# Kernel optimization log

Measured on AMD Instinct MI355X. Metric: run time of the kernel, lower is better.

Reference implementation:

```python
import jax, jax.numpy as jnp
import numpy as np

B_, N_, D_ = 2, 2048, 512
E_ = 2 * D_          # d_inner = expand * dim
S_ = 16              # d_state
K_ = 4               # d_conv
R_ = 32              # dt_rank = ceil(dim/16)
C_ = 512             # cond_dim


def setup_inputs() -> dict:
    key = jax.random.key(0)
    ks = jax.random.split(key, 12)
    r = lambda i, sh, s=0.02: jax.random.normal(ks[i], sh, dtype=jnp.float32) * s
    return {
        "x": jax.random.normal(ks[0], (B_, N_, D_), dtype=jnp.float32),
        "cond": jax.random.normal(ks[1], (B_, C_), dtype=jnp.float32),
        "ln_g": jnp.ones((D_,), jnp.float32),
        "ln_b": jnp.zeros((D_,), jnp.float32),
        "W_in": r(2, (D_, 2 * E_)),            # in_proj (no bias)
        "conv_w": r(3, (E_, K_), 0.1),          # depthwise causal conv
        "conv_b": jnp.zeros((E_,), jnp.float32),
        "W_x": r(4, (E_, R_ + 2 * S_)),         # x_proj -> dt,B,C
        "W_dt": r(5, (R_, E_), 0.1),
        "b_dt": jnp.full((E_,), -4.6, jnp.float32),  # softplus(-4.6)~0.01
        "A_log": jnp.log(jnp.broadcast_to(jnp.arange(1, S_ + 1, dtype=jnp.float32), (E_, S_))),
        "D_skip": jnp.ones((E_,), jnp.float32),
        "W_out": r(6, (E_, D_)),                # out_proj (no bias)
        "film_gw": r(7, (C_, D_)),
        "film_gb": jnp.ones((D_,), jnp.float32),
        "film_bw": r(8, (C_, D_)),
        "film_bb": jnp.zeros((D_,), jnp.float32),
    }


def reference(x, cond, ln_g, ln_b, W_in, conv_w, conv_b, W_x, W_dt, b_dt,
              A_log, D_skip, W_out, film_gw, film_gb, film_bw, film_bb):
    # --- LayerNorm ---
    mu = x.mean(-1, keepdims=True)
    var = ((x - mu) ** 2).mean(-1, keepdims=True)
    xn = (x - mu) * jax.lax.rsqrt(var + 1e-5) * ln_g + ln_b

    # --- Mamba ---
    xz = xn @ W_in                                  # [B,N,2E]
    u, z = jnp.split(xz, 2, axis=-1)                # [B,N,E] each
    # causal depthwise conv1d (kernel K_), unrolled over small K
    up = jnp.pad(u, ((0, 0), (K_ - 1, 0), (0, 0)))
    uc = conv_b + sum(up[:, k:k + N_, :] * conv_w[:, k] for k in range(K_))
    uc = jax.nn.silu(uc)                            # [B,N,E]

    x_dbl = uc @ W_x                                # [B,N,R+2S]
    dt, Bm, Cm = jnp.split(x_dbl, [R_, R_ + S_], axis=-1)
    delta = jax.nn.softplus(dt @ W_dt + b_dt)       # [B,N,E]

    A = -jnp.exp(A_log)                             # [E,S]
    dA = jnp.exp(delta[..., None] * A)              # [B,N,E,S]
    dBu = (delta * uc)[..., None] * Bm[:, :, None, :]  # [B,N,E,S]

    def step(h, ins):
        dA_t, dBu_t, C_t = ins                      # [B,E,S],[B,E,S],[B,S]
        h = dA_t * h + dBu_t
        y = jnp.einsum('bes,bs->be', h, C_t)
        return h, y

    h0 = jnp.zeros((x.shape[0], E_, S_), dtype=x.dtype)
    _, ys = jax.lax.scan(step, h0,
                         (dA.swapaxes(0, 1), dBu.swapaxes(0, 1), Cm.swapaxes(0, 1)))
    y = ys.swapaxes(0, 1) + D_skip * uc             # [B,N,E]
    y = y * jax.nn.silu(z)
    out = y @ W_out                                 # [B,N,D]

    # --- FiLM ---
    gamma = cond @ film_gw + film_gb                # [B,D]
    beta = cond @ film_bw + film_bb
    return gamma[:, None, :] * out + beta[:, None, :]
```

## Files before the change

kernel.cpp:

```cpp
#include <hip/hip_runtime.h>
#include <hip/hip_bf16.h>
#include <math.h>

#define B_ 2
#define N_ 2048
#define D_ 512
#define E_ 1024
#define S_ 16
#define R_ 32
#define C_ 512
#define CH_ 32
#define NC_ (N_ / CH_)

using short8 = __attribute__((ext_vector_type(8))) short;
using f32x4  = __attribute__((ext_vector_type(4))) float;
using f32x16 = __attribute__((ext_vector_type(16))) float;

__device__ __forceinline__ short f2bf(float f) {
    union { float f; unsigned u; } x; x.f = f;
    unsigned r = (x.u + 0x7fffu + ((x.u >> 16) & 1u)) >> 16;
    return (short)r;
}
__device__ __forceinline__ float bf2f(short s) {
    union { unsigned u; float f; } x;
    x.u = ((unsigned)(unsigned short)s) << 16;
    return x.f;
}
__device__ __forceinline__ void gl_lds16(const void* g, void* l) {
    __builtin_amdgcn_global_load_lds((const __attribute__((address_space(1))) void*)g,
                                     (__attribute__((address_space(3))) void*)l, 16, 0, 0);
}

__device__ __forceinline__ void transpose32(const float* __restrict__ W, short* __restrict__ Wt,
                                            int K, int N, int bx, int by, float (*t)[33], int tid) {
    int n0 = bx * 32, k0 = by * 32;
    int c = tid & 31, rr0 = tid >> 5;
#pragma unroll
    for (int rr = rr0; rr < 32; rr += 8)
        t[rr][c] = W[(size_t)(k0 + rr) * N + n0 + c];
    __syncthreads();
#pragma unroll
    for (int rr = rr0; rr < 32; rr += 8)
        Wt[(size_t)(n0 + rr) * K + k0 + c] = f2bf(t[c][rr]);
}

__global__ __launch_bounds__(256) void prep1_kernel(
    const float* __restrict__ x, short* __restrict__ xnb,
    const float* __restrict__ lng, const float* __restrict__ lnb,
    const float* __restrict__ W_in, short* __restrict__ Wint) {
    __shared__ __align__(16) float smem[32 * 33];
    int bid = blockIdx.x;
    int tid = threadIdx.x;
    if (bid < 1024) {
        int t = bid * 4 + (tid >> 6);
        int lane = tid & 63;
        const float* src = x + (size_t)t * D_ + lane * 8;
        float4 v0 = *(const float4*)src;
        float4 v1 = *(const float4*)(src + 4);
        float s = v0.x + v0.y + v0.z + v0.w + v1.x + v1.y + v1.z + v1.w;
        float s2 = v0.x * v0.x;
        s2 = fmaf(v0.y, v0.y, s2); s2 = fmaf(v0.z, v0.z, s2); s2 = fmaf(v0.w, v0.w, s2);
        s2 = fmaf(v1.x, v1.x, s2); s2 = fmaf(v1.y, v1.y, s2);
        s2 = fmaf(v1.z, v1.z, s2); s2 = fmaf(v1.w, v1.w, s2);
#pragma unroll
        for (int o = 32; o >= 1; o >>= 1) {
            s += __shfl_xor(s, o);
            s2 += __shfl_xor(s2, o);
        }
        float mu = s * (1.f / (float)D_);
        float var = s2 * (1.f / (float)D_) - mu * mu;
        float rs = rsqrtf(var + 1e-5f);
        float4 g0 = *(const float4*)(lng + lane * 8);
        float4 g1 = *(const float4*)(lng + lane * 8 + 4);
        float4 b0 = *(const float4*)(lnb + lane * 8);
        float4 b1 = *(const float4*)(lnb + lane * 8 + 4);
        short8 o;
        o[0] = f2bf((v0.x - mu) * rs * g0.x + b0.x);
        o[1] = f2bf((v0.y - mu) * rs * g0.y + b0.y);
        o[2] = f2bf((v0.z - mu) * rs * g0.z + b0.z);
        o[3] = f2bf((v0.w - mu) * rs * g0.w + b0.w);
        o[4] = f2bf((v1.x - mu) * rs * g1.x + b1.x);
        o[5] = f2bf((v1.y - mu) * rs * g1.y + b1.y);
        o[6] = f2bf((v1.z - mu) * rs * g1.z + b1.z);
        o[7] = f2bf((v1.w - mu) * rs * g1.w + b1.w);
        *(short8*)(xnb + (size_t)t * D_ + lane * 8) = o;
    } else {
        int r = bid - 1024;
        transpose32(W_in, Wint, 512, 2048, r % 64, r / 64, (float(*)[33])smem, tid);
    }
}

__global__ __launch_bounds__(256) void gemm1_hybrid(
    const short* __restrict__ A, const short* __restrict__ Bt, short* __restrict__ Cb,
    const float* __restrict__ W_out, short* __restrict__ Woutt,
    const float* __restrict__ W_x, short* __restrict__ Wxt,
    const float* __restrict__ W_dt, short* __restrict__ Wdtt,
    const float* __restrict__ cond,
    const float* __restrict__ gw, const float* __restrict__ gb,
    const float* __restrict__ bw, const float* __restrict__ bb,
    float* __restrict__ gamma, float* __restrict__ beta) {
    __shared__ __align__(16) char smem[32768];
    int bid = blockIdx.x;
    int tid = threadIdx.x;
    if (bid < 512) {
        constexpr int BM = 128, BN = 128, BK = 64;
        constexpr int M = 4096, N = 2048, K = 512;
        short* As = (short*)smem;
        short* Bs = As + BM * BK;
        int lane = tid & 63, w = tid >> 6;
        int wr = w >> 1, wc = w & 1;
        int swz = (bid & 7) * 64 + (bid >> 3);
        int m0 = (swz >> 4) * BM, n0 = (swz & 15) * BN;
        int lr = lane >> 3, lc = lane & 7;
        f32x16 acc[2][2];
#pragma unroll
        for (int i = 0; i < 2; i++)
#pragma unroll
            for (int j = 0; j < 2; j++)
#pragma unroll
                for (int r = 0; r < 16; r++) acc[i][j][r] = 0.f;
        int l31 = lane & 31, hk = (lane >> 5) * 8;
        for (int k0 = 0; k0 < K; k0 += BK) {
            __syncthreads();
#pragma unroll
            for (int ch = w; ch < BM / 8; ch += 4)
                gl_lds16(&A[(size_t)(m0 + ch * 8 + lr) * K + k0 + lc * 8], &As[ch * 512]);
#pragma unroll
            for (int ch = w; ch < BN / 8; ch += 4)
                gl_lds16(&Bt[(size_t)(n0 + ch * 8 + lr) * K + k0 + lc * 8], &Bs[ch * 512]);
            __syncthreads();
#pragma unroll
            for (int kk = 0; kk < 4; kk++) {
                short8 a[2], b[2];
#pragma unroll
                for (int i = 0; i < 2; i++)
                    a[i] = *(const short8*)&As[(wr * 64 + i * 32 + l31) * BK + kk * 16 + hk];
#pragma unroll
                for (int j = 0; j < 2; j++)
                    b[j] = *(const short8*)&Bs[(wc * 64 + j * 32 + l31) * BK + kk * 16 + hk];
#pragma unroll
                for (int i = 0; i < 2; i++)
#pragma unroll
                    for (int j = 0; j < 2; j++)
                        acc[i][j] = __builtin_amdgcn_mfma_f32_32x32x16_bf16(a[i], b[j], acc[i][j], 0, 0, 0);
            }
        }
        int rbase = 4 * (lane >> 5);
#pragma unroll
        for (int i = 0; i < 2; i++)
#pragma unroll
            for (int j = 0; j < 2; j++) {
                int col = n0 + wc * 64 + j * 32 + l31;
#pragma unroll
                for (int r = 0; r < 16; r++) {
                    int row = m0 + wr * 64 + i * 32 + rbase + (r & 3) + 8 * (r >> 2);
                    Cb[(size_t)row * N + col] = f2bf(acc[i][j][r]);
                }
            }
    } else if (bid < 520) {
        float* cs = (float*)smem;
        float* red = (float*)smem + 1024;
        int d0 = (bid - 512) * 64;
#pragma unroll
        for (int i = tid; i < 2 * C_ / 4; i += 256) {
            int b = i >> 7;
            int c4 = (i & 127) * 4;
            *(float4*)&cs[b * C_ + c4] = *(const float4*)(cond + (size_t)b * C_ + c4);
        }
        __syncthreads();
        int dl = tid & 63, ks = tid >> 6;
        int d = d0 + dl;
        float g0 = 0.f, g1 = 0.f, bt0 = 0.f, bt1 = 0.f;
#pragma unroll 4
        for (int k = ks * 128; k < ks * 128 + 128; k++) {
            float wg = gw[(size_t)k * D_ + d];
            float wb = bw[(size_t)k * D_ + d];
            float c0 = cs[k], c1 = cs[C_ + k];
            g0 = fmaf(c0, wg, g0);
            g1 = fmaf(c1, wg, g1);
            bt0 = fmaf(c0, wb, bt0);
            bt1 = fmaf(c1, wb, bt1);
        }
        red[(ks * 64 + dl) * 4 + 0] = g0; red[(ks * 64 + dl) * 4 + 1] = g1;
        red[(ks * 64 + dl) * 4 + 2] = bt0; red[(ks * 64 + dl) * 4 + 3] = bt1;
        __syncthreads();
        if (ks == 0) {
            float s0 = 0.f, s1 = 0.f, s2 = 0.f, s3 = 0.f;
#pragma unroll
            for (int q = 0; q < 4; q++) {
                s0 += red[(q * 64 + dl) * 4 + 0]; s1 += red[(q * 64 + dl) * 4 + 1];
                s2 += red[(q * 64 + dl) * 4 + 2]; s3 += red[(q * 64 + dl) * 4 + 3];
            }
            float gbv = gb[d], bbv = bb[d];
            gamma[d] = s0 + gbv;
            gamma[D_ + d] = s1 + gbv;
            beta[d] = s2 + bbv;
            beta[D_ + d] = s3 + bbv;
        }
    } else if (bid < 1032) {
        int r = bid - 520;
        transpose32(W_out, Woutt, 1024, 512, r % 16, r / 16, (float(*)[33])smem, tid);
    } else if (bid < 1096) {
        int r = bid - 1032;
        transpose32(W_x, Wxt, 1024, 64, r % 2, r / 2, (float(*)[33])smem, tid);
    } else {
        int r = bid - 1096;
        transpose32(W_dt, Wdtt, 32, 1024, r, 0, (float(*)[33])smem, tid);
    }
}

template <int BM, int BN>
__global__ __launch_bounds__(256) void gemm2_kernel(
    const short* __restrict__ A, const short* __restrict__ Bt, float* __restrict__ Cf,
    int M, int N, int K,
    const float* __restrict__ gamma, const float* __restrict__ beta) {
    constexpr int BK = 64;
    constexpr int WM = BM / 2, WN = BN / 2;
    constexpr int MR = WM / 32, NR = WN / 32;
    __shared__ __align__(16) short As[BM * BK];
    __shared__ __align__(16) short Bs[BN * BK];
    int tid = threadIdx.x;
    int lane = tid & 63, w = tid >> 6;
    int wr = w >> 1, wc = w & 1;
    int lid = blockIdx.x;
    int chunk = gridDim.x >> 3;
    int swz = (lid & 7) * chunk + (lid >> 3);
    int ntiles = N / BN;
    int m0 = (swz / ntiles) * BM, n0 = (swz % ntiles) * BN;
    int lr = lane >> 3, lc = lane & 7;

    f32x16 acc[MR][NR];
#pragma unroll
    for (int i = 0; i < MR; i++)
#pragma unroll
        for (int j = 0; j < NR; j++)
#pragma unroll
            for (int r = 0; r < 16; r++) acc[i][j][r] = 0.f;

    int l31 = lane & 31, hk = (lane >> 5) * 8;

    for (int k0 = 0; k0 < K; k0 += BK) {
        __syncthreads();
#pragma unroll
        for (int ch = w; ch < BM / 8; ch += 4)
            gl_lds16(&A[(size_t)(m0 + ch * 8 + lr) * K + k0 + lc * 8], &As[ch * 512]);
#pragma unroll
        for (int ch = w; ch < BN / 8; ch += 4)
            gl_lds16(&Bt[(size_t)(n0 + ch * 8 + lr) * K + k0 + lc * 8], &Bs[ch * 512]);
        __syncthreads();
#pragma unroll
        for (int kk = 0; kk < 4; kk++) {
            short8 a[MR], b[NR];
#pragma unroll
            for (int i = 0; i < MR; i++)
                a[i] = *(const short8*)&As[(wr * WM + i * 32 + l31) * BK + kk * 16 + hk];
#pragma unroll
            for (int j = 0; j < NR; j++)
                b[j] = *(const short8*)&Bs[(wc * WN + j * 32 + l31) * BK + kk * 16 + hk];
#pragma unroll
            for (int i = 0; i < MR; i++)
#pragma unroll
                for (int j = 0; j < NR; j++)
                    acc[i][j] = __builtin_amdgcn_mfma_f32_32x32x16_bf16(a[i], b[j], acc[i][j], 0, 0, 0);
        }
    }
    int rbase = 4 * (lane >> 5);
    int bi = m0 >> 11;
#pragma unroll
    for (int i = 0; i < MR; i++)
#pragma unroll
        for (int j = 0; j < NR; j++) {
            int col = n0 + wc * WN + j * 32 + l31;
            float gm = gamma[bi * D_ + col];
            float bt = beta[bi * D_ + col];
#pragma unroll
            for (int r = 0; r < 16; r++) {
                int row = m0 + wr * WM + i * 32 + rbase + (r & 3) + 8 * (r >> 2);
                Cf[(size_t)row * N + col] = gm * acc[i][j][r] + bt;
            }
        }
}

__global__ __launch_bounds__(512) void mid_kernel(
    const short* __restrict__ xzb, const float* __restrict__ cw, const float* __restrict__ cb,
    const short* __restrict__ Wxt,
    const short* __restrict__ Wdtt,
    const float* __restrict__ bdt,
    short* __restrict__ ucb, float* __restrict__ xdbl, short* __restrict__ deltab) {
    constexpr int LDU = 1032;
    __shared__ __align__(16) short u[16 * LDU];
    __shared__ __align__(16) float xd2[2][16 * 68];
    int tid = threadIdx.x;
    int t0 = blockIdx.x * 16;
    int n0 = t0 & (N_ - 1);
    {
        int c8 = (tid & 127) * 8;
        int base = (tid >> 7) * 4;
        float4 wv[8];
        float cbv[8];
#pragma unroll
        for (int j = 0; j < 8; j++) {
            wv[j] = *(const float4*)(cw + (c8 + j) * 4);
            cbv[j] = cb[c8 + j];
        }
        float uf[7][8];
#pragma unroll
        for (int j = 0; j < 7; j++) {
            short8 v = {0, 0, 0, 0, 0, 0, 0, 0};
            if (n0 + base - 3 + j >= 0)
                v = *(const short8*)&xzb[(size_t)(t0 + base - 3 + j) * (2 * E_) + c8];
#pragma unroll
            for (int q = 0; q < 8; q++) uf[j][q] = bf2f(v[q]);
        }
#pragma unroll
        for (int k = 0; k < 4; k++) {
            int n = base + k;
            short8 o;
#pragma unroll
            for (int q = 0; q < 8; q++) {
                float a = fmaf(wv[q].x, uf[k][q],
                          fmaf(wv[q].y, uf[k + 1][q],
                          fmaf(wv[q].z, uf[k + 2][q],
                          fmaf(wv[q].w, uf[k + 3][q], cbv[q]))));
                float v = a / (1.f + __expf(-a));
                o[q] = f2bf(v);
            }
            *(short8*)&ucb[(size_t)(t0 + n) * E_ + c8] = o;
            *(short8*)&u[n * LDU + c8] = o;
        }
    }
    __syncthreads();
    int lane = tid & 63, w = tid >> 6;
    int cg = w & 3, kh = w >> 2;
    int l15 = lane & 15, kq = (lane >> 4) * 8;
    f32x4 acc4 = {0.f, 0.f, 0.f, 0.f};
#pragma unroll 8
    for (int k0 = 0; k0 < 16; k0++) {
        int kk = kh * 512 + k0 * 32;
        short8 af = *(const short8*)&u[l15 * LDU + kk + kq];
        short8 bfr = *(const short8*)&Wxt[(size_t)(cg * 16 + l15) * E_ + kk + kq];
        acc4 = __builtin_amdgcn_mfma_f32_16x16x32_bf16(af, bfr, acc4, 0, 0, 0);
    }
#pragma unroll
    for (int j = 0; j < 4; j++)
        xd2[kh][((lane >> 4) * 4 + j) * 68 + cg * 16 + l15] = acc4[j];
    __syncthreads();
    if (tid < 256) {
        int r = tid >> 4, c4 = (tid & 15) * 4;
        float4 a = *(const float4*)&xd2[0][r * 68 + c4];
        float4 b = *(const float4*)&xd2[1][r * 68 + c4];
        a.x += b.x; a.y += b.y; a.z += b.z; a.w += b.w;
        *(float4*)&xd2[0][r * 68 + c4] = a;
        *(float4*)&xdbl[(size_t)(t0 + r) * 64 + c4] = a;
    }
    __syncthreads();
    float av[8];
    *(float4*)&av[0] = *(const float4*)&xd2[0][l15 * 68 + kq];
    *(float4*)&av[4] = *(const float4*)&xd2[0][l15 * 68 + kq + 4];
    short8 ab;
#pragma unroll
    for (int j = 0; j < 8; j++) ab[j] = f2bf(av[j]);
    int row4 = (lane >> 4) * 4;
#pragma unroll 4
    for (int t = 0; t < 8; t++) {
        int e = w * 128 + t * 16 + l15;
        short8 bb = *(const short8*)&Wdtt[(size_t)e * 32 + kq];
        f32x4 c4v = {0.f, 0.f, 0.f, 0.f};
        c4v = __builtin_amdgcn_mfma_f32_16x16x32_bf16(ab, bb, c4v, 0, 0, 0);
        float bv = bdt[e];
#pragma unroll
        for (int j = 0; j < 4; j++) {
            float xv = c4v[j] + bv;
            float sp = (xv > 20.f) ? xv : log1pf(__expf(xv));
            deltab[(size_t)(t0 + row4 + j) * E_ + e] = f2bf(sp);
        }
    }
}

__global__ __launch_bounds__(256) void scan_p1(const short* __restrict__ deltab,
                                               const short* __restrict__ ucb,
                                               const float* __restrict__ xdbl,
                                               const float* __restrict__ A_log,
                                               short* __restrict__ hend,
                                               float* __restrict__ cumd) {
    int blk = blockIdx.x;
    int eq = blk & 3;
    int c = (blk >> 2) & (NC_ - 1);
    int b = blk >> 8;
    int tid = threadIdx.x;
    int e = eq * 256 + tid;
    __shared__ float Bsl[CH_][16];
    int base = (b * N_ + c * CH_) * 64;
    for (int i = tid; i < CH_ * 16; i += 256) {
        int n = i >> 4, col = i & 15;
        Bsl[n][col] = xdbl[base + n * 64 + R_ + col];
    }
    float Aes[16];
    const float4* al = (const float4*)(A_log + e * 16);
#pragma unroll
    for (int j = 0; j < 4; j++) {
        float4 a = al[j];
        Aes[j * 4 + 0] = -__expf(a.x);
        Aes[j * 4 + 1] = -__expf(a.y);
        Aes[j * 4 + 2] = -__expf(a.z);
        Aes[j * 4 + 3] = -__expf(a.w);
    }
    __syncthreads();
    float h[16];
#pragma unroll
    for (int s = 0; s < 16; s++) h[s] = 0.f;
    float cum = 0.f;
    const short* dp = deltab + (size_t)(b * N_ + c * CH_) * E_ + e;
    const short* up = ucb + (size_t)(b * N_ + c * CH_) * E_ + e;
#pragma unroll 2
    for (int n = 0; n < CH_; n++) {
        float dv = bf2f(dp[n * E_]);
        float uv = bf2f(up[n * E_]);
        float du = dv * uv;
        cum += dv;
        float Bl[16];
#pragma unroll
        for (int j = 0; j < 4; j++) *(float4*)&Bl[j * 4] = *(const float4*)&Bsl[n][j * 4];
#pragma unroll
        for (int s = 0; s < 16; s++) {
            float dA = __expf(dv * Aes[s]);
            h[s] = fmaf(dA, h[s], du * Bl[s]);
        }
    }
    size_t ob = (size_t)(b * NC_ + c) * 16 * E_ + e;
#pragma unroll
    for (int s = 0; s < 16; s++) hend[ob + (size_t)s * E_] = f2bf(h[s]);
    cumd[(size_t)(b * NC_ + c) * E_ + e] = cum;
}

__global__ __launch_bounds__(256) void scan_comb(short* __restrict__ hend,
                                                 const float* __restrict__ cumd,
                                                 const float* __restrict__ A_log) {
    __shared__ float lh[64][65];
    __shared__ float lp[64][65];
    int blk = blockIdx.x;
    int et = blk & 15;
    int s = (blk >> 4) & 15;
    int b = blk >> 8;
    int e0 = et * 64;
    int tid = threadIdx.x;
    int lane = tid & 63, w = tid >> 6;
    for (int i = tid; i < 64 * 64; i += 256) {
        int c = i >> 6, e = i & 63;
        lh[c][e] = bf2f(hend[((size_t)((b * NC_ + c) * 16) + s) * E_ + e0 + e]);
        lp[c][e] = cumd[(size_t)(b * NC_ + c) * E_ + e0 + e];
    }
    __syncthreads();
#pragma unroll 4
    for (int q = 0; q < 16; q++) {
        int e = w * 16 + q;
        float Aes = -__expf(A_log[(e0 + e) * 16 + s]);
        float A = __expf(Aes * lp[lane][e]);
        float Bv = lh[lane][e];
#pragma unroll
        for (int off = 1; off < 64; off <<= 1) {
            float Ap = __shfl_up(A, off);
            float Bp = __shfl_up(Bv, off);
            if (lane >= off) {
                Bv = fmaf(A, Bp, Bv);
                A *= Ap;
            }
        }
        float hB = __shfl_up(Bv, 1);
        lh[lane][e] = (lane == 0) ? 0.f : hB;
    }
    __syncthreads();
    for (int i = tid; i < 64 * 64; i += 256) {
        int c = i >> 6, e = i & 63;
        hend[((size_t)((b * NC_ + c) * 16) + s) * E_ + e0 + e] = f2bf(lh[c][e]);
    }
}

__global__ __launch_bounds__(256) void scan_p3(const short* __restrict__ deltab,
                                               const short* __restrict__ ucb,
                                               const float* __restrict__ xdbl,
                                               const short* __restrict__ xzb,
                                               const float* __restrict__ A_log,
                                               const float* __restrict__ D_skip,
                                               const short* __restrict__ hend,
                                               short* __restrict__ yb) {
    int blk = blockIdx.x;
    int eq = blk & 3;
    int c = (blk >> 2) & (NC_ - 1);
    int b = blk >> 8;
    int tid = threadIdx.x;
    int e = eq * 256 + tid;
    __shared__ float Bsl[CH_][16];
    __shared__ float Csl[CH_][16];
    int base = (b * N_ + c * CH_) * 64;
    for (int i = tid; i < CH_ * 32; i += 256) {
        int n = i >> 5, col = i & 31;
        float v = xdbl[base + n * 64 + R_ + col];
        if (col < 16) Bsl[n][col] = v;
        else Csl[n][col - 16] = v;
    }
    float Aes[16];
    const float4* al = (const float4*)(A_log + e * 16);
#pragma unroll
    for (int j = 0; j < 4; j++) {
        float4 a = al[j];
        Aes[j * 4 + 0] = -__expf(a.x);
        Aes[j * 4 + 1] = -__expf(a.y);
        Aes[j * 4 + 2] = -__expf(a.z);
        Aes[j * 4 + 3] = -__expf(a.w);
    }
    float dsk = D_skip[e];
    float h[16];
    size_t ob = (size_t)(b * NC_ + c) * 16 * E_ + e;
#pragma unroll
    for (int s = 0; s < 16; s++) h[s] = bf2f(hend[ob + (size_t)s * E_]);
    __syncthreads();
    const short* dp = deltab + (size_t)(b * N_ + c * CH_) * E_ + e;
    const short* up = ucb + (size_t)(b * N_ + c * CH_) * E_ + e;
    const short* zp = xzb + (size_t)(b * N_ + c * CH_) * (2 * E_) + E_ + e;
    short* yp = yb + (size_t)(b * N_ + c * CH_) * E_ + e;
#pragma unroll 2
    for (int n = 0; n < CH_; n++) {
        float dv = bf2f(dp[n * E_]);
        float uv = bf2f(up[n * E_]);
        float du = dv * uv;
        float Bl[16], Cl[16];
#pragma unroll
        for (int j = 0; j < 4; j++) {
            *(float4*)&Bl[j * 4] = *(const float4*)&Bsl[n][j * 4];
            *(float4*)&Cl[j * 4] = *(const float4*)&Csl[n][j * 4];
        }
        float y = 0.f;
#pragma unroll
        for (int s = 0; s < 16; s++) {
            float dA = __expf(dv * Aes[s]);
            h[s] = fmaf(dA, h[s], du * Bl[s]);
            y = fmaf(h[s], Cl[s], y);
        }
        float zv = bf2f(zp[n * 2 * E_]);
        float yy = y + dsk * uv;
        yy = yy * (zv / (1.f + __expf(-zv)));
        yp[n * E_] = f2bf(yy);
    }
}

extern "C" void kernel_launch(void* const* d_in, const int* in_sizes, int n_in,
                              void* d_out, int out_size, void* d_ws, size_t ws_size,
                              hipStream_t stream) {
    const float* x       = (const float*)d_in[0];
    const float* cond    = (const float*)d_in[1];
    const float* ln_g    = (const float*)d_in[2];
    const float* ln_b    = (const float*)d_in[3];
    const float* W_in    = (const float*)d_in[4];
    const float* conv_w  = (const float*)d_in[5];
    const float* conv_b  = (const float*)d_in[6];
    const float* W_x     = (const float*)d_in[7];
    const float* W_dt    = (const float*)d_in[8];
    const float* b_dt    = (const float*)d_in[9];
    const float* A_log   = (const float*)d_in[10];
    const float* D_skip  = (const float*)d_in[11];
    const float* W_out   = (const float*)d_in[12];
    const float* film_gw = (const float*)d_in[13];
    const float* film_gb = (const float*)d_in[14];
    const float* film_bw = (const float*)d_in[15];
    const float* film_bb = (const float*)d_in[16];
    float* out = (float*)d_out;

    float* ws = (float*)d_ws;
    float* xdbl  = ws;
    float* gamma = xdbl + 262144;
    float* beta  = gamma + 1024;
    float* cumd  = beta + 1024;
    short* hend  = (short*)(cumd + 131072);
    short* xzb   = hend + 2097152;
    short* ucb   = xzb + 8388608;
    short* deltab = ucb + 4194304;
    short* Wint  = deltab + 4194304;
    short* Woutt = Wint + 1048576;
    short* yb    = Woutt + 524288;
    short* Wxt   = yb + 4194304;
    short* Wdtt  = Wxt + 65536;
    short* xnb   = Wdtt + 32768;

    prep1_kernel<<<2048, 256, 0, stream>>>(x, xnb, ln_g, ln_b, W_in, Wint);

    gemm1_hybrid<<<1128, 256, 0, stream>>>(
        xnb, Wint, xzb, W_out, Woutt, W_x, Wxt, W_dt, Wdtt,
        cond, film_gw, film_gb, film_bw, film_bb, gamma, beta);

    mid_kernel<<<B_ * N_ / 16, 512, 0, stream>>>(
        xzb, conv_w, conv_b, Wxt, Wdtt, b_dt, ucb, xdbl, deltab);

    scan_p1<<<B_ * NC_ * 4, 256, 0, stream>>>(deltab, ucb, xdbl, A_log, hend, cumd);
    scan_comb<<<B_ * S_ * (E_ / 64), 256, 0, stream>>>(hend, cumd, A_log);
    scan_p3<<<B_ * NC_ * 4, 256, 0, stream>>>(deltab, ucb, xdbl, xzb, A_log, D_skip, hend, yb);

    gemm2_kernel<64, 64>
        <<<512, 256, 0, stream>>>(
            yb, Woutt, out, B_ * N_, D_, E_, gamma, beta);
}
```

Baseline: 128.5 us.

## Fuse chunked scan pass 1 into mid_kernel with finer 16-step chunks

Removes the separate scan_p1 kernel. Each mid_kernel block now computes per-chunk local state and cumulative delta for its own 16 tokens, reusing the u and B values already in shared memory. This doubles the number of chunks, so scan_comb now processes 128 chunks per batch with two chunks per lane, and scan_p3 reads the combined state at every other fine chunk. The change saves a launch and re-reading delta, u and B from global memory. In exchange, the scan work is serialized inside mid_kernel and the hend/cumd traffic doubles.

After: 130.9 us. Within noise of the previous version (+1.9%).

```diff
diff --git a/kernel.cpp b/kernel.cpp
--- a/kernel.cpp
+++ b/kernel.cpp
@@ -10,7 +10,8 @@
 #define R_ 32
 #define C_ 512
 #define CH_ 32
-#define NC_ (N_ / CH_)
+#define NC_ 64
+#define FC_ 128
 
 using short8 = __attribute__((ext_vector_type(8))) short;
 using f32x4  = __attribute__((ext_vector_type(4))) float;
@@ -104,7 +105,7 @@
     int tid = threadIdx.x;
     if (bid < 512) {
         constexpr int BM = 128, BN = 128, BK = 64;
-        constexpr int M = 4096, N = 2048, K = 512;
+        constexpr int N = 2048, K = 512;
         short* As = (short*)smem;
         short* Bs = As + BM * BK;
         int lane = tid & 63, w = tid >> 6;
@@ -285,8 +286,9 @@
     const short* __restrict__ xzb, const float* __restrict__ cw, const float* __restrict__ cb,
     const short* __restrict__ Wxt,
     const short* __restrict__ Wdtt,
-    const float* __restrict__ bdt,
-    short* __restrict__ ucb, float* __restrict__ xdbl, short* __restrict__ deltab) {
+    const float* __restrict__ bdt, const float* __restrict__ A_log,
+    short* __restrict__ ucb, float* __restrict__ xdbl, short* __restrict__ deltab,
+    short* __restrict__ hend, float* __restrict__ cumd) {
     constexpr int LDU = 1032;
     __shared__ __align__(16) short u[16 * LDU];
     __shared__ __align__(16) float xd2[2][16 * 68];
@@ -354,109 +356,95 @@
         *(float4*)&xdbl[(size_t)(t0 + r) * 64 + c4] = a;
     }
     __syncthreads();
-    float av[8];
-    *(float4*)&av[0] = *(const float4*)&xd2[0][l15 * 68 + kq];
-    *(float4*)&av[4] = *(const float4*)&xd2[0][l15 * 68 + kq + 4];
-    short8 ab;
-#pragma unroll
-    for (int j = 0; j < 8; j++) ab[j] = f2bf(av[j]);
-    int row4 = (lane >> 4) * 4;
+    {
+        float av[8];
+        *(float4*)&av[0] = *(const float4*)&xd2[0][l15 * 68 + kq];
+        *(float4*)&av[4] = *(const float4*)&xd2[0][l15 * 68 + kq + 4];
+        short8 ab;
+#pragma unroll
+        for (int j = 0; j < 8; j++) ab[j] = f2bf(av[j]);
+        int row4 = (lane >> 4) * 4;
 #pragma unroll 4
-    for (int t = 0; t < 8; t++) {
-        int e = w * 128 + t * 16 + l15;
-        short8 bb = *(const short8*)&Wdtt[(size_t)e * 32 + kq];
-        f32x4 c4v = {0.f, 0.f, 0.f, 0.f};
-        c4v = __builtin_amdgcn_mfma_f32_16x16x32_bf16(ab, bb, c4v, 0, 0, 0);
-        float bv = bdt[e];
+        for (int t = 0; t < 8; t++) {
+            int e = w * 128 + t * 16 + l15;
+            short8 bb = *(const short8*)&Wdtt[(size_t)e * 32 + kq];
+            f32x4 c4v = {0.f, 0.f, 0.f, 0.f};
+            c4v = __builtin_amdgcn_mfma_f32_16x16x32_bf16(ab, bb, c4v, 0, 0, 0);
+            float bv = bdt[e];
+#pragma unroll
+            for (int j = 0; j < 4; j++) {
+                float xv = c4v[j] + bv;
+                float sp = (xv > 20.f) ? xv : log1pf(__expf(xv));
+                deltab[(size_t)(t0 + row4 + j) * E_ + e] = f2bf(sp);
+            }
+        }
+    }
+    __syncthreads();
+#pragma unroll
+    for (int half = 0; half < 2; half++) {
+        int e = tid + half * 512;
+        float Aes[16];
+        const float4* al = (const float4*)(A_log + e * 16);
 #pragma unroll
         for (int j = 0; j < 4; j++) {
-            float xv = c4v[j] + bv;
-            float sp = (xv > 20.f) ? xv : log1pf(__expf(xv));
-            deltab[(size_t)(t0 + row4 + j) * E_ + e] = f2bf(sp);
-        }
-    }
-}
-
-__global__ __launch_bounds__(256) void scan_p1(const short* __restrict__ deltab,
-                                               const short* __restrict__ ucb,
-                                               const float* __restrict__ xdbl,
-                                               const float* __restrict__ A_log,
-                                               short* __restrict__ hend,
-                                               float* __restrict__ cumd) {
-    int blk = blockIdx.x;
-    int eq = blk & 3;
-    int c = (blk >> 2) & (NC_ - 1);
-    int b = blk >> 8;
-    int tid = threadIdx.x;
-    int e = eq * 256 + tid;
-    __shared__ float Bsl[CH_][16];
-    int base = (b * N_ + c * CH_) * 64;
-    for (int i = tid; i < CH_ * 16; i += 256) {
-        int n = i >> 4, col = i & 15;
-        Bsl[n][col] = xdbl[base + n * 64 + R_ + col];
-    }
-    float Aes[16];
-    const float4* al = (const float4*)(A_log + e * 16);
-#pragma unroll
-    for (int j = 0; j < 4; j++) {
-        float4 a = al[j];
-        Aes[j * 4 + 0] = -__expf(a.x);
-        Aes[j * 4 + 1] = -__expf(a.y);
-        Aes[j * 4 + 2] = -__expf(a.z);
-        Aes[j * 4 + 3] = -__expf(a.w);
-    }
-    __syncthreads();
-    float h[16];
-#pragma unroll
-    for (int s = 0; s < 16; s++) h[s] = 0.f;
-    float cum = 0.f;
-    const short* dp = deltab + (size_t)(b * N_ + c * CH_) * E_ + e;
-    const short* up = ucb + (size_t)(b * N_ + c * CH_) * E_ + e;
+            float4 a = al[j];
+            Aes[j * 4 + 0] = -__expf(a.x);
+            Aes[j * 4 + 1] = -__expf(a.y);
+            Aes[j * 4 + 2] = -__expf(a.z);
+            Aes[j * 4 + 3] = -__expf(a.w);
+        }
+        float h[16];
+#pragma unroll
+        for (int s = 0; s < 16; s++) h[s] = 0.f;
+        float cum = 0.f;
 #pragma unroll 2
-    for (int n = 0; n < CH_; n++) {
-        float dv = bf2f(dp[n * E_]);
-        float uv = bf2f(up[n * E_]);
-        float du = dv * uv;
-        cum += dv;
-        float Bl[16];
-#pragma unroll
-        for (int j = 0; j < 4; j++) *(float4*)&Bl[j * 4] = *(const float4*)&Bsl[n][j * 4];
-#pragma unroll
-        for (int s = 0; s < 16; s++) {
-            float dA = __expf(dv * Aes[s]);
-            h[s] = fmaf(dA, h[s], du * Bl[s]);
-        }
-    }
-    size_t ob = (size_t)(b * NC_ + c) * 16 * E_ + e;
-#pragma unroll
-    for (int s = 0; s < 16; s++) hend[ob + (size_t)s * E_] = f2bf(h[s]);
-    cumd[(size_t)(b * NC_ + c) * E_ + e] = cum;
+        for (int n = 0; n < 16; n++) {
+            float dv = bf2f(deltab[(size_t)(t0 + n) * E_ + e]);
+            float uv = bf2f(u[n * LDU + e]);
+            float du = dv * uv;
+            cum += dv;
+#pragma unroll
+            for (int s = 0; s < 16; s++) {
+                float dA = __expf(dv * Aes[s]);
+                h[s] = fmaf(dA, h[s], du * xd2[0][n * 68 + 32 + s]);
+            }
+        }
+#pragma unroll
+        for (int s = 0; s < 16; s++)
+            hend[((size_t)blockIdx.x * 16 + s) * E_ + e] = f2bf(h[s]);
+        cumd[(size_t)blockIdx.x * E_ + e] = cum;
+    }
 }
 
 __global__ __launch_bounds__(256) void scan_comb(short* __restrict__ hend,
                                                  const float* __restrict__ cumd,
                                                  const float* __restrict__ A_log) {
-    __shared__ float lh[64][65];
-    __shared__ float lp[64][65];
+    __shared__ float lh[FC_][33];
+    __shared__ float lp[FC_][33];
     int blk = blockIdx.x;
-    int et = blk & 15;
-    int s = (blk >> 4) & 15;
-    int b = blk >> 8;
-    int e0 = et * 64;
+    int et = blk & 31;
+    int s = (blk >> 5) & 15;
+    int b = blk >> 9;
+    int e0 = et * 32;
     int tid = threadIdx.x;
     int lane = tid & 63, w = tid >> 6;
-    for (int i = tid; i < 64 * 64; i += 256) {
-        int c = i >> 6, e = i & 63;
-        lh[c][e] = bf2f(hend[((size_t)((b * NC_ + c) * 16) + s) * E_ + e0 + e]);
-        lp[c][e] = cumd[(size_t)(b * NC_ + c) * E_ + e0 + e];
-    }
-    __syncthreads();
-#pragma unroll 4
-    for (int q = 0; q < 16; q++) {
-        int e = w * 16 + q;
+    for (int i = tid; i < FC_ * 32; i += 256) {
+        int c = i >> 5, e = i & 31;
+        lh[c][e] = bf2f(hend[((size_t)((b * FC_ + c) * 16) + s) * E_ + e0 + e]);
+        lp[c][e] = cumd[(size_t)(b * FC_ + c) * E_ + e0 + e];
+    }
+    __syncthreads();
+#pragma unroll
+    for (int q = 0; q < 8; q++) {
+        int e = w * 8 + q;
         float Aes = -__expf(A_log[(e0 + e) * 16 + s]);
-        float A = __expf(Aes * lp[lane][e]);
-        float Bv = lh[lane][e];
+        int c0 = 2 * lane, c1 = c0 + 1;
+        float A0 = __expf(Aes * lp[c0][e]);
+        float B0 = lh[c0][e];
+        float A1 = __expf(Aes * lp[c1][e]);
+        float B1 = lh[c1][e];
+        float A = A1 * A0;
+        float Bv = fmaf(A1, B0, B1);
 #pragma unroll
         for (int off = 1; off < 64; off <<= 1) {
             float Ap = __shfl_up(A, off);
@@ -466,13 +454,15 @@
                 A *= Ap;
             }
         }
-        float hB = __shfl_up(Bv, 1);
-        lh[lane][e] = (lane == 0) ? 0.f : hB;
-    }
-    __syncthreads();
-    for (int i = tid; i < 64 * 64; i += 256) {
-        int c = i >> 6, e = i & 63;
-        hend[((size_t)((b * NC_ + c) * 16) + s) * E_ + e0 + e] = f2bf(lh[c][e]);
+        float pB = __shfl_up(Bv, 1);
+        if (lane == 0) pB = 0.f;
+        lh[c0][e] = pB;
+        lh[c1][e] = fmaf(A0, pB, B0);
+    }
+    __syncthreads();
+    for (int i = tid; i < FC_ * 32; i += 256) {
+        int c = i >> 5, e = i & 31;
+        hend[((size_t)((b * FC_ + c) * 16) + s) * E_ + e0 + e] = f2bf(lh[c][e]);
     }
 }
 
@@ -511,7 +501,7 @@
     }
     float dsk = D_skip[e];
     float h[16];
-    size_t ob = (size_t)(b * NC_ + c) * 16 * E_ + e;
+    size_t ob = (size_t)((b * FC_ + c * 2) * 16) * E_ + e;
 #pragma unroll
     for (int s = 0; s < 16; s++) h[s] = bf2f(hend[ob + (size_t)s * E_]);
     __syncthreads();
@@ -571,8 +561,8 @@
     float* gamma = xdbl + 262144;
     float* beta  = gamma + 1024;
     float* cumd  = beta + 1024;
-    short* hend  = (short*)(cumd + 131072);
-    short* xzb   = hend + 2097152;
+    short* hend  = (short*)(cumd + 262144);
+    short* xzb   = hend + 4194304;
     short* ucb   = xzb + 8388608;
     short* deltab = ucb + 4194304;
     short* Wint  = deltab + 4194304;
@@ -589,10 +579,10 @@
         cond, film_gw, film_gb, film_bw, film_bb, gamma, beta);
 
     mid_kernel<<<B_ * N_ / 16, 512, 0, stream>>>(
-        xzb, conv_w, conv_b, Wxt, Wdtt, b_dt, ucb, xdbl, deltab);
-
-    scan_p1<<<B_ * NC_ * 4, 256, 0, stream>>>(deltab, ucb, xdbl, A_log, hend, cumd);
-    scan_comb<<<B_ * S_ * (E_ / 64), 256, 0, stream>>>(hend, cumd, A_log);
+        xzb, conv_w, conv_b, Wxt, Wdtt, b_dt, A_log, ucb, xdbl, deltab, hend, cumd);
+
+    scan_comb<<<B_ * S_ * 32, 256, 0, stream>>>(hend, cumd, A_log);
+
     scan_p3<<<B_ * NC_ * 4, 256, 0, stream>>>(deltab, ucb, xdbl, xzb, A_log, D_skip, hend, yb);
 
     gemm2_kernel<64, 64>
```
